# Kernel optimization log

Hardware: AMD Instinct MI355X
Metric: run time of the kernel (lower is better)

## Reference

```python
import jax, jax.numpy as jnp
import numpy as np

DIM = 768
NUM_HEADS = 12
HEAD_DIM = DIM // NUM_HEADS  # 64
IMG_W = 32
IMG_H = 32
B = 16
N = IMG_W * IMG_H + 1  # 1025 (CLS + grid)


def setup_inputs() -> dict:
    key = jax.random.key(0)
    k1, k2, k3, k4, k5 = jax.random.split(key, 5)
    x = jax.random.normal(k1, (B, N, DIM), dtype=jnp.float32)
    W_qkv = jax.random.normal(k2, (3 * DIM, DIM), dtype=jnp.float32) * 0.02
    W_proj = jax.random.normal(k3, (DIM, DIM), dtype=jnp.float32) * 0.02
    b_proj = jax.random.normal(k4, (DIM,), dtype=jnp.float32) * 0.02
    # learned mixed-RoPE frequencies, shape (2, num_heads * head_dim//2)
    freqs = jax.random.normal(k5, (2, NUM_HEADS * (HEAD_DIM // 2)), dtype=jnp.float32) * 0.1
    return {"x": x, "W_qkv": W_qkv, "W_proj": W_proj, "b_proj": b_proj, "freqs": freqs}


def _mixed_angles(freqs):
    # t_x = t % W, t_y = t // W over the flattened grid (init_t_xy)
    t = jnp.arange(IMG_W * IMG_H, dtype=jnp.float32)
    t_x = t % IMG_W
    t_y = jnp.floor(t / IMG_W)
    # outer products -> (N-1, H, hd/2) -> (H, N-1, hd/2); angle = fx + fy
    fx = (t_x[:, None] * freqs[0][None, :]).reshape(-1, NUM_HEADS, HEAD_DIM // 2)
    fy = (t_y[:, None] * freqs[1][None, :]).reshape(-1, NUM_HEADS, HEAD_DIM // 2)
    return (fx + fy).transpose(1, 0, 2)  # (H, N-1, hd/2)


def _apply_rope(t, cos, sin):
    # t: (B, H, N-1, hd); complex multiply on (even, odd) pairs
    pairs = t.reshape(*t.shape[:-1], HEAD_DIM // 2, 2)
    x0, x1 = pairs[..., 0], pairs[..., 1]
    o0 = x0 * cos - x1 * sin
    o1 = x0 * sin + x1 * cos
    return jnp.stack([o0, o1], axis=-1).reshape(t.shape)


def reference(x, W_qkv, W_proj, b_proj, freqs):
    Bx, Nx, C = x.shape
    scale = HEAD_DIM ** -0.5
    qkv = jnp.einsum('bnc,dc->bnd', x, W_qkv)  # Linear, no bias
    qkv = qkv.reshape(Bx, Nx, 3, NUM_HEADS, HEAD_DIM).transpose(2, 0, 3, 1, 4)
    q, k, v = qkv[0], qkv[1], qkv[2]  # (B, H, N, hd)

    ang = _mixed_angles(freqs)  # (H, N-1, hd/2)
    cos, sin = jnp.cos(ang), jnp.sin(ang)  # broadcast over batch

    # rotate all tokens except the leading CLS token
    q = jnp.concatenate([q[:, :, :1], _apply_rope(q[:, :, 1:], cos, sin)], axis=2)
    k = jnp.concatenate([k[:, :, :1], _apply_rope(k[:, :, 1:], cos, sin)], axis=2)

    attn = jax.nn.softmax(jnp.einsum('bhqd,bhkd->bhqk', q * scale, k), axis=-1)
    out = jnp.einsum('bhqk,bhkd->bhqd', attn, v)  # (B, H, N, hd)
    out = out.transpose(0, 2, 1, 3).reshape(Bx, Nx, C)
    return out @ W_proj.T + b_proj
```

## Files before the change

kernel.cpp:

```cpp
#include <hip/hip_runtime.h>
#include <math.h>

#define DIM     768
#define NH      12
#define HD      64
#define NTOK    1025
#define BATCH   16
#define MTOT    (BATCH * NTOK)
#define QKVD    (3 * DIM)

typedef short  short8 __attribute__((ext_vector_type(8)));
typedef float  f32x4  __attribute__((ext_vector_type(4)));

typedef const __attribute__((address_space(1))) void gvoid_t;
typedef __attribute__((address_space(3)))       void lvoid_t;
#define GLD16(gsrc, ldst) __builtin_amdgcn_global_load_lds( \
    (gvoid_t*)(gsrc), (lvoid_t*)(ldst), 16, 0, 0)

static __device__ __forceinline__ unsigned int f2bf(float f) {
    unsigned int u = __float_as_uint(f);
    u += 0x7FFFu + ((u >> 16) & 1u);
    return u >> 16;
}

static __device__ __forceinline__ float red_sum(float x) {
    x += __shfl_xor(x, 16);
    x += __shfl_xor(x, 32);
    return x;
}

__device__ __forceinline__ void cvt8(const float* __restrict__ src,
                                     unsigned short* __restrict__ dst, int i) {
    float4 a = *(const float4*)(src + (size_t)i*8);
    float4 b = *(const float4*)(src + (size_t)i*8 + 4);
    uint4 pk;
    pk.x = f2bf(a.x) | (f2bf(a.y) << 16);
    pk.y = f2bf(a.z) | (f2bf(a.w) << 16);
    pk.z = f2bf(b.x) | (f2bf(b.y) << 16);
    pk.w = f2bf(b.z) | (f2bf(b.w) << 16);
    *(uint4*)(dst + (size_t)i*8) = pk;
}

__global__ __launch_bounds__(256) void cvt_bf16_kernel(
    const float* __restrict__ x, const float* __restrict__ Wq,
    const float* __restrict__ Wp,
    unsigned short* __restrict__ xb, unsigned short* __restrict__ Wqb,
    unsigned short* __restrict__ Wpb)
{
    const int stride = gridDim.x * blockDim.x;
    const int tid = blockIdx.x * blockDim.x + threadIdx.x;
    for (int i = tid; i < MTOT*DIM/8;  i += stride) cvt8(x,  xb,  i);
    for (int i = tid; i < QKVD*DIM/8;  i += stride) cvt8(Wq, Wqb, i);
    for (int i = tid; i < DIM*DIM/8;   i += stride) cvt8(Wp, Wpb, i);
}

__global__ __launch_bounds__(256) void rope_tab_kernel(
    const float* __restrict__ freqs, float2* __restrict__ tab)
{
    const int gid = blockIdx.x * 256 + threadIdx.x;
    const int p  = gid & 31;
    const int n1 = (gid >> 5) & 1023;
    const int h  = gid >> 15;
    const float tx = (float)(n1 & 31), ty = (float)(n1 >> 5);
    const float ang = tx * freqs[h*32 + p] + ty * freqs[384 + h*32 + p];
    float s, c;
    sincosf(ang, &s, &c);
    tab[gid] = make_float2(c, s);
}

__device__ __forceinline__ void gemm_core(
    const unsigned short* __restrict__ Wb,
    const unsigned short* __restrict__ Xb,
    int D0, int T0, int maxXrow,
    short* Ws, short* Xs, f32x4 acc[4][4], int tid)
{
    const int lane = tid & 63;
    const int wu   = __builtin_amdgcn_readfirstlane(tid >> 6);
    const int wr   = wu >> 1, wc = wu & 1;
    const int l4   = lane >> 4, l15 = lane & 15;

    const int srow = lane >> 3;
    const int schk = (lane & 7) ^ srow;
    const unsigned short* wsrc[4];
    const unsigned short* xsrc[4];
#pragma unroll
    for (int i = 0; i < 4; ++i) {
        int r = wu*32 + i*8 + srow;
        wsrc[i] = Wb + (size_t)(D0 + r) * DIM + schk*8;
        int xr = T0 + r; if (xr > maxXrow) xr = maxXrow;
        xsrc[i] = Xb + (size_t)xr * DIM + schk*8;
    }

    for (int kt = 0; kt < DIM/64; ++kt) {
        __syncthreads();
#pragma unroll
        for (int i = 0; i < 4; ++i) {
            GLD16(wsrc[i] + kt*64, &Ws[(wu*4 + i) * 512]);
            GLD16(xsrc[i] + kt*64, &Xs[(wu*4 + i) * 512]);
        }
        __syncthreads();

        short8 wf[4][2], xf[4][2];
#pragma unroll
        for (int f = 0; f < 4; ++f) {
            const int rw = wr*64 + f*16 + l15;
            const int rx = wc*64 + f*16 + l15;
#pragma unroll
            for (int kf = 0; kf < 2; ++kf) {
                wf[f][kf] = *(const short8*)&Ws[rw*64 + (((kf*4 + l4) ^ (rw & 7)) << 3)];
                xf[f][kf] = *(const short8*)&Xs[rx*64 + (((kf*4 + l4) ^ (rx & 7)) << 3)];
            }
        }
        __builtin_amdgcn_s_setprio(1);
#pragma unroll
        for (int kf = 0; kf < 2; ++kf)
#pragma unroll
            for (int fm = 0; fm < 4; ++fm)
#pragma unroll
                for (int fn = 0; fn < 4; ++fn)
                    acc[fm][fn] = __builtin_amdgcn_mfma_f32_16x16x32_bf16(
                        wf[fm][kf], xf[fn][kf], acc[fm][fn], 0, 0, 0);
        __builtin_amdgcn_s_setprio(0);
    }
}

__global__ __launch_bounds__(256) void qkv_gemm_kernel(
    const unsigned short* __restrict__ Wqb, const unsigned short* __restrict__ xb,
    const float2* __restrict__ tab,
    unsigned short* __restrict__ Qb, unsigned short* __restrict__ Kb,
    unsigned short* __restrict__ Vb)
{
    __shared__ __align__(16) short Ws[128*64];
    __shared__ __align__(16) short Xs[128*64];
    f32x4 acc[4][4] = {};
    const int tid = threadIdx.x;
    const int D0 = blockIdx.x * 128;
    const int T0 = blockIdx.y * 128;
    gemm_core(Wqb, xb, D0, T0, MTOT - 1, Ws, Xs, acc, tid);

    const int lane = tid & 63;
    const int wu = tid >> 6, wr = wu >> 1, wc = wu & 1;
    const int l4 = lane >> 4, l15 = lane & 15;
    const int which = D0 / DIM;
    unsigned short* dst = (which == 0) ? Qb : (which == 1) ? Kb : Vb;
    const float qs = (which == 0) ? 0.125f * 1.44269504089f : 1.f;

    unsigned bArr[4], nArr[4];
    bool vArr[4];
#pragma unroll
    for (int fn = 0; fn < 4; ++fn) {
        unsigned m = T0 + wc*64 + fn*16 + l15;
        vArr[fn] = m < MTOT;
        bArr[fn] = m / NTOK;
        nArr[fn] = m - bArr[fn]*NTOK;
    }
#pragma unroll
    for (int fm = 0; fm < 4; ++fm) {
        const int hcol = (D0 % DIM) + wr*64 + fm*16 + l4*4;
        const int h = hcol >> 6, dd = hcol & 63;
        const int p0 = dd >> 1;
#pragma unroll
        for (int fn = 0; fn < 4; ++fn) {
            if (!vArr[fn]) continue;
            f32x4 a = acc[fm][fn];
            const int n = nArr[fn];
            if (which < 2) {
                int n1 = n > 0 ? n - 1 : 0;
                float4 cs = *(const float4*)&tab[(size_t)(h*1024 + n1)*32 + p0];
                if (n == 0) cs = make_float4(1.f, 0.f, 1.f, 0.f);
                float e0 = a[0], od0 = a[1], e1 = a[2], od1 = a[3];
                a[0] = e0*cs.x - od0*cs.y;  a[1] = e0*cs.y + od0*cs.x;
                a[2] = e1*cs.z - od1*cs.w;  a[3] = e1*cs.w + od1*cs.z;
            }
            uint2 pk;
            pk.x = f2bf(a[0]*qs) | (f2bf(a[1]*qs) << 16);
            pk.y = f2bf(a[2]*qs) | (f2bf(a[3]*qs) << 16);
            *(uint2*)&dst[((size_t)(bArr[fn]*NH + h)*NTOK + n)*HD + dd] = pk;
        }
    }
}

__global__ __launch_bounds__(256) void attn_mfma_kernel(
    const unsigned short* __restrict__ Qb,
    const unsigned short* __restrict__ Kb,
    const unsigned short* __restrict__ Vb,
    unsigned short* __restrict__ Obf)
{
    __shared__ __align__(16) char KsR[2][8192];
    __shared__ __align__(16) char VtR[2][8192];
    __shared__ __align__(16) char PsR[4][4096];

    const int tid  = threadIdx.x;
    const int lane = tid & 63;
    const int w    = __builtin_amdgcn_readfirstlane(tid >> 6);
    const int l4   = lane >> 4, l15 = lane & 15, l7 = lane & 7;

    const int d    = blockIdx.x;
    const int xcd  = d & 7;
    const int s    = d >> 3;
    const int bh   = xcd * 24 + s / 9;
    const int q0   = (s % 9) * 128;
    const size_t base = (size_t)bh * NTOK * HD;

    short8 qf[2][2];
#pragma unroll
    for (int qg = 0; qg < 2; ++qg) {
        int qr = q0 + w*32 + qg*16 + l15;
        int qrc = qr < NTOK ? qr : NTOK - 1;
        qf[qg][0] = *(const short8*)(Qb + base + (size_t)qrc*HD + l4*8);
        qf[qg][1] = *(const short8*)(Qb + base + (size_t)qrc*HD + 32 + l4*8);
    }

    float lA = 0.f, lB = 0.f;
    f32x4 oA[4] = {}, oB[4] = {};

    const int ktokb = tid >> 3;
    const int kchk  = tid & 7;
    const int vtok  = ((tid & 7) << 3) | ((tid >> 3) & 7);
    const int vc    = vtok >> 3;
    const int vb2   = (vtok & 7) * 2;
    char* Pw = &PsR[w][0];

    uint4 vg[2];
#pragma unroll
    for (int i = 0; i < 2; ++i)
        vg[i] = *(const uint4*)(Vb + base + (size_t)vtok*HD + w*8 + i*32);
#pragma unroll
    for (int i = 0; i < 2; ++i) {
        int tok = ktokb + i*32;
        int sc = kchk ^ (tok & 7);
        GLD16(Kb + base + (size_t)tok*HD + sc*8, &KsR[0][w*1024 + i*4096]);
    }
#pragma unroll
    for (int i = 0; i < 2; ++i) {
        const int vd0 = w*8 + i*32;
        unsigned short vs[8];
        vs[0]=(unsigned short)vg[i].x; vs[1]=(unsigned short)(vg[i].x>>16);
        vs[2]=(unsigned short)vg[i].y; vs[3]=(unsigned short)(vg[i].y>>16);
        vs[4]=(unsigned short)vg[i].z; vs[5]=(unsigned short)(vg[i].z>>16);
        vs[6]=(unsigned short)vg[i].w; vs[7]=(unsigned short)(vg[i].w>>16);
#pragma unroll
        for (int j = 0; j < 8; ++j)
            *(unsigned short*)(&VtR[0][0] + (vd0+j)*128 + ((vc ^ j) << 4) + vb2) = vs[j];
    }
#pragma unroll
    for (int i = 0; i < 2; ++i) {
        int gv = 64 + vtok;
        vg[i] = (gv < NTOK)
            ? *(const uint4*)(Vb + base + (size_t)gv*HD + w*8 + i*32)
            : make_uint4(0,0,0,0);
    }

    for (int kt = 0; kt < 17; ++kt) {
        const int buf = kt & 1;
        __syncthreads();

        if (kt < 16) {
            const int nb = buf ^ 1;
#pragma unroll
            for (int i = 0; i < 2; ++i) {
                int tok = ktokb + i*32;
                int gk = (kt+1)*64 + tok; if (gk > NTOK-1) gk = NTOK-1;
                int sc = kchk ^ (tok & 7);
                GLD16(Kb + base + (size_t)gk*HD + sc*8, &KsR[nb][w*1024 + i*4096]);
            }
#pragma unroll
            for (int i = 0; i < 2; ++i) {
                const int vd0 = w*8 + i*32;
                unsigned short vs[8];
                vs[0]=(unsigned short)vg[i].x; vs[1]=(unsigned short)(vg[i].x>>16);
                vs[2]=(unsigned short)vg[i].y; vs[3]=(unsigned short)(vg[i].y>>16);
                vs[4]=(unsigned short)vg[i].z; vs[5]=(unsigned short)(vg[i].z>>16);
                vs[6]=(unsigned short)vg[i].w; vs[7]=(unsigned short)(vg[i].w>>16);
#pragma unroll
                for (int j = 0; j < 8; ++j)
                    *(unsigned short*)(&VtR[nb][0] + (vd0+j)*128 + ((vc ^ j) << 4) + vb2) = vs[j];
            }
            const int ktn = (kt+2 < 17) ? kt+2 : 16;
#pragma unroll
            for (int i = 0; i < 2; ++i) {
                int gv = ktn*64 + vtok;
                vg[i] = (gv < NTOK)
                    ? *(const uint4*)(Vb + base + (size_t)gv*HD + w*8 + i*32)
                    : make_uint4(0,0,0,0);
            }
        }

        f32x4 sA[4] = {}, sB[4] = {};
        __builtin_amdgcn_s_setprio(1);
#pragma unroll
        for (int tg = 0; tg < 4; ++tg) {
            const int row = tg*16 + l15;
            short8 ka0 = *(const short8*)(&KsR[buf][0] + row*128 + ((l4 ^ l7) << 4));
            short8 ka1 = *(const short8*)(&KsR[buf][0] + row*128 + (((4 + l4) ^ l7) << 4));
            sA[tg] = __builtin_amdgcn_mfma_f32_16x16x32_bf16(ka0, qf[0][0], sA[tg], 0,0,0);
            sA[tg] = __builtin_amdgcn_mfma_f32_16x16x32_bf16(ka1, qf[0][1], sA[tg], 0,0,0);
            sB[tg] = __builtin_amdgcn_mfma_f32_16x16x32_bf16(ka0, qf[1][0], sB[tg], 0,0,0);
            sB[tg] = __builtin_amdgcn_mfma_f32_16x16x32_bf16(ka1, qf[1][1], sB[tg], 0,0,0);
        }
        __builtin_amdgcn_s_setprio(0);

        float pA[16], pB[16];
        if (kt == 16) {
#pragma unroll
            for (int tg = 0; tg < 4; ++tg)
#pragma unroll
                for (int r = 0; r < 4; ++r) {
                    int tok = 1024 + tg*16 + l4*4 + r;
                    float sa = (tok > 1024) ? -3e38f : sA[tg][r];
                    float sb = (tok > 1024) ? -3e38f : sB[tg][r];
                    pA[tg*4+r] = __builtin_exp2f(sa);
                    pB[tg*4+r] = __builtin_exp2f(sb);
                }
        } else {
#pragma unroll
            for (int tg = 0; tg < 4; ++tg)
#pragma unroll
                for (int r = 0; r < 4; ++r) {
                    pA[tg*4+r] = __builtin_exp2f(sA[tg][r]);
                    pB[tg*4+r] = __builtin_exp2f(sB[tg][r]);
                }
        }
        float psA = 0.f, psB = 0.f;
#pragma unroll
        for (int i = 0; i < 16; ++i) { psA += pA[i]; psB += pB[i]; }
        lA += psA;
        lB += psB;

#pragma unroll
        for (int tg = 0; tg < 4; ++tg) {
            unsigned k0a, k1a, k0b, k1b;
            asm volatile("v_cvt_pk_bf16_f32 %0, %1, %2" : "=v"(k0a) : "v"(pA[tg*4+0]), "v"(pA[tg*4+1]));
            asm volatile("v_cvt_pk_bf16_f32 %0, %1, %2" : "=v"(k1a) : "v"(pA[tg*4+2]), "v"(pA[tg*4+3]));
            asm volatile("v_cvt_pk_bf16_f32 %0, %1, %2" : "=v"(k0b) : "v"(pB[tg*4+0]), "v"(pB[tg*4+1]));
            asm volatile("v_cvt_pk_bf16_f32 %0, %1, %2" : "=v"(k1b) : "v"(pB[tg*4+2]), "v"(pB[tg*4+3]));
            const int chk = (((tg*2 + (l4 >> 1)) ^ l7) << 4) + (l4 & 1)*8;
            *(uint2*)(Pw + l15*128      + chk) = make_uint2(k0a, k1a);
            *(uint2*)(Pw + (16+l15)*128 + chk) = make_uint2(k0b, k1b);
        }
        __builtin_amdgcn_wave_barrier();

        const short8 pf00 = *(const short8*)(Pw + l15*128      + ((l4 ^ l7) << 4));
        const short8 pf01 = *(const short8*)(Pw + l15*128      + (((4+l4) ^ l7) << 4));
        const short8 pf10 = *(const short8*)(Pw + (16+l15)*128 + ((l4 ^ l7) << 4));
        const short8 pf11 = *(const short8*)(Pw + (16+l15)*128 + (((4+l4) ^ l7) << 4));

        __builtin_amdgcn_s_setprio(1);
#pragma unroll
        for (int dg = 0; dg < 4; ++dg) {
            const int dd = dg*16 + l15;
            short8 v0 = *(const short8*)(&VtR[buf][0] + dd*128 + ((l4 ^ (dd & 7)) << 4));
            short8 v1 = *(const short8*)(&VtR[buf][0] + dd*128 + (((4 + l4) ^ (dd & 7)) << 4));
            oA[dg] = __builtin_amdgcn_mfma_f32_16x16x32_bf16(v0, pf00, oA[dg], 0,0,0);
            oA[dg] = __builtin_amdgcn_mfma_f32_16x16x32_bf16(v1, pf01, oA[dg], 0,0,0);
            oB[dg] = __builtin_amdgcn_mfma_f32_16x16x32_bf16(v0, pf10, oB[dg], 0,0,0);
            oB[dg] = __builtin_amdgcn_mfma_f32_16x16x32_bf16(v1, pf11, oB[dg], 0,0,0);
        }
        __builtin_amdgcn_s_setprio(0);
    }

    const float liA = 1.f / red_sum(lA);
    const float liB = 1.f / red_sum(lB);
    const int b = bh / NH, h = bh % NH;
    const int qA = q0 + w*32 + l15;
    const int qB = qA + 16;
    if (qA < NTOK) {
        unsigned short* p = Obf + ((size_t)b*NTOK + qA)*DIM + h*HD + l4*4;
#pragma unroll
        for (int dg = 0; dg < 4; ++dg) {
            uint2 pk;
            pk.x = f2bf(oA[dg][0]*liA) | (f2bf(oA[dg][1]*liA) << 16);
            pk.y = f2bf(oA[dg][2]*liA) | (f2bf(oA[dg][3]*liA) << 16);
            *(uint2*)(p + dg*16) = pk;
        }
    }
    if (qB < NTOK) {
        unsigned short* p = Obf + ((size_t)b*NTOK + qB)*DIM + h*HD + l4*4;
#pragma unroll
        for (int dg = 0; dg < 4; ++dg) {
            uint2 pk;
            pk.x = f2bf(oB[dg][0]*liB) | (f2bf(oB[dg][1]*liB) << 16);
            pk.y = f2bf(oB[dg][2]*liB) | (f2bf(oB[dg][3]*liB) << 16);
            *(uint2*)(p + dg*16) = pk;
        }
    }
}

__global__ __launch_bounds__(256) void proj_gemm_kernel(
    const unsigned short* __restrict__ Wpb, const unsigned short* __restrict__ Obf,
    const float* __restrict__ bp, float* __restrict__ out)
{
    __shared__ __align__(16) short Ws[128*64];
    __shared__ __align__(16) short Xs[128*64];
    f32x4 acc[4][4] = {};
    const int tid = threadIdx.x;
    const int D0 = blockIdx.x * 128;
    const int T0 = blockIdx.y * 128;
    gemm_core(Wpb, Obf, D0, T0, MTOT - 1, Ws, Xs, acc, tid);

    const int lane = tid & 63;
    const int wu = tid >> 6, wr = wu >> 1, wc = wu & 1;
    const int l4 = lane >> 4, l15 = lane & 15;

    unsigned mArr[4];
    bool vArr[4];
#pragma unroll
    for (int fn = 0; fn < 4; ++fn) {
        unsigned m = T0 + wc*64 + fn*16 + l15;
        mArr[fn] = m;
        vArr[fn] = m < MTOT;
    }
#pragma unroll
    for (int fm = 0; fm < 4; ++fm) {
        const int nG = D0 + wr*64 + fm*16 + l4*4;
        const float4 bias = *(const float4*)&bp[nG];
#pragma unroll
        for (int fn = 0; fn < 4; ++fn) {
            if (!vArr[fn]) continue;
            f32x4 a = acc[fm][fn];
            float4 v = make_float4(a[0]+bias.x, a[1]+bias.y, a[2]+bias.z, a[3]+bias.w);
            *(float4*)&out[(size_t)mArr[fn]*DIM + nG] = v;
        }
    }
}

extern "C" void kernel_launch(void* const* d_in, const int* in_sizes, int n_in,
                              void* d_out, int out_size, void* d_ws, size_t ws_size,
                              hipStream_t stream)
{
    const float* x     = (const float*)d_in[0];
    const float* Wqkv  = (const float*)d_in[1];
    const float* Wp    = (const float*)d_in[2];
    const float* bp    = (const float*)d_in[3];
    const float* freqs = (const float*)d_in[4];
    float* out = (float*)d_out;

    const size_t SZ = (size_t)BATCH * NH * NTOK * HD;
    unsigned short* Qb  = (unsigned short*)d_ws;
    unsigned short* Kb  = Qb + SZ;
    unsigned short* Vb  = Kb + SZ;
    unsigned short* Obf = Vb + SZ;
    unsigned short* xb  = Obf + SZ;
    unsigned short* Wqb = xb + SZ;
    unsigned short* Wpb = Wqb + (size_t)QKVD * DIM;
    float2*         tab = (float2*)(Wpb + (size_t)DIM * DIM);

    cvt_bf16_kernel<<<2048, 256, 0, stream>>>(x, Wqkv, Wp, xb, Wqb, Wpb);
    rope_tab_kernel<<<1536, 256, 0, stream>>>(freqs, tab);
    qkv_gemm_kernel<<<dim3(QKVD/128, (MTOT + 127)/128), 256, 0, stream>>>(
        Wqb, xb, tab, Qb, Kb, Vb);
    attn_mfma_kernel<<<1728, 256, 0, stream>>>(Qb, Kb, Vb, Obf);
    proj_gemm_kernel<<<dim3(DIM/128, (MTOT + 127)/128), 256, 0, stream>>>(
        Wpb, Obf, bp, out);
}
```

Before: 279.6 us.

## Pad Q/K/V token dimension to 1088 with zeros to drop attention tail masking

```diff
diff --git a/kernel.cpp b/kernel.cpp
--- a/kernel.cpp
+++ b/kernel.cpp
@@ -5,6 +5,7 @@
 #define NH      12
 #define HD      64
 #define NTOK    1025
+#define NTOKP   1088
 #define BATCH   16
 #define MTOT    (BATCH * NTOK)
 #define QKVD    (3 * DIM)
@@ -66,6 +67,19 @@
     float s, c;
     sincosf(ang, &s, &c);
     tab[gid] = make_float2(c, s);
+}
+
+__global__ __launch_bounds__(256) void pad_zero_kernel(
+    unsigned short* __restrict__ Qb, unsigned short* __restrict__ Kb,
+    unsigned short* __restrict__ Vb)
+{
+    const int gid   = blockIdx.x * 256 + threadIdx.x;
+    const int which = gid / 96768;
+    const int r     = gid - which * 96768;
+    const int bh    = r / 504;
+    const int off   = r - bh * 504;
+    unsigned short* p = (which == 0) ? Qb : (which == 1) ? Kb : Vb;
+    *(uint4*)(p + ((size_t)bh*NTOKP + NTOK)*HD + off*8) = make_uint4(0,0,0,0);
 }
 
 __device__ __forceinline__ void gemm_core(
@@ -175,7 +189,7 @@
             uint2 pk;
             pk.x = f2bf(a[0]*qs) | (f2bf(a[1]*qs) << 16);
             pk.y = f2bf(a[2]*qs) | (f2bf(a[3]*qs) << 16);
-            *(uint2*)&dst[((size_t)(bArr[fn]*NH + h)*NTOK + n)*HD + dd] = pk;
+            *(uint2*)&dst[((size_t)(bArr[fn]*NH + h)*NTOKP + n)*HD + dd] = pk;
         }
     }
 }
@@ -186,8 +200,8 @@
     const unsigned short* __restrict__ Vb,
     unsigned short* __restrict__ Obf)
 {
-    __shared__ __align__(16) char KsR[2][8192];
-    __shared__ __align__(16) char VtR[2][8192];
+    __shared__ __align__(16) char KsR[2*8192];
+    __shared__ __align__(16) char VtR[2*8192];
     __shared__ __align__(16) char PsR[4][4096];
 
     const int tid  = threadIdx.x;
@@ -200,7 +214,7 @@
     const int s    = d >> 3;
     const int bh   = xcd * 24 + s / 9;
     const int q0   = (s % 9) * 128;
-    const size_t base = (size_t)bh * NTOK * HD;
+    const size_t base = (size_t)bh * NTOKP * HD;
 
     short8 qf[2][2];
 #pragma unroll
@@ -221,16 +235,19 @@
     const int vb2   = (vtok & 7) * 2;
     char* Pw = &PsR[w][0];
 
+    const unsigned short* kp0 = Kb + base + (size_t)ktokb*HD
+                                + (size_t)(kchk ^ (ktokb & 7))*8;
+    const unsigned short* kp1 = kp0 + 32*HD;
+    const unsigned short* vp  = Vb + base + (size_t)vtok*HD + w*8;
+
+    GLD16(kp0, KsR + w*1024);
+    GLD16(kp1, KsR + 4096 + w*1024);
+    kp0 += 4096; kp1 += 4096;
+
     uint4 vg[2];
-#pragma unroll
-    for (int i = 0; i < 2; ++i)
-        vg[i] = *(const uint4*)(Vb + base + (size_t)vtok*HD + w*8 + i*32);
-#pragma unroll
-    for (int i = 0; i < 2; ++i) {
-        int tok = ktokb + i*32;
-        int sc = kchk ^ (tok & 7);
-        GLD16(Kb + base + (size_t)tok*HD + sc*8, &KsR[0][w*1024 + i*4096]);
-    }
+    vg[0] = *(const uint4*)vp;
+    vg[1] = *(const uint4*)(vp + 32);
+    vp += 4096;
 #pragma unroll
     for (int i = 0; i < 2; ++i) {
         const int vd0 = w*8 + i*32;
@@ -241,29 +258,24 @@
         vs[6]=(unsigned short)vg[i].w; vs[7]=(unsigned short)(vg[i].w>>16);
 #pragma unroll
         for (int j = 0; j < 8; ++j)
-            *(unsigned short*)(&VtR[0][0] + (vd0+j)*128 + ((vc ^ j) << 4) + vb2) = vs[j];
-    }
-#pragma unroll
-    for (int i = 0; i < 2; ++i) {
-        int gv = 64 + vtok;
-        vg[i] = (gv < NTOK)
-            ? *(const uint4*)(Vb + base + (size_t)gv*HD + w*8 + i*32)
-            : make_uint4(0,0,0,0);
-    }
+            *(unsigned short*)(VtR + (vd0+j)*128 + ((vc ^ j) << 4) + vb2) = vs[j];
+    }
+    vg[0] = *(const uint4*)vp;
+    vg[1] = *(const uint4*)(vp + 32);
+    vp += 4096;
 
     for (int kt = 0; kt < 17; ++kt) {
         const int buf = kt & 1;
+        const char* Kc = KsR + buf*8192;
+        const char* Vc = VtR + buf*8192;
         __syncthreads();
 
         if (kt < 16) {
-            const int nb = buf ^ 1;
-#pragma unroll
-            for (int i = 0; i < 2; ++i) {
-                int tok = ktokb + i*32;
-                int gk = (kt+1)*64 + tok; if (gk > NTOK-1) gk = NTOK-1;
-                int sc = kchk ^ (tok & 7);
-                GLD16(Kb + base + (size_t)gk*HD + sc*8, &KsR[nb][w*1024 + i*4096]);
-            }
+            char* kd = KsR + (buf^1)*8192 + w*1024;
+            GLD16(kp0, kd);
+            GLD16(kp1, kd + 4096);
+            kp0 += 4096; kp1 += 4096;
+            char* vd = VtR + (buf^1)*8192;
 #pragma unroll
             for (int i = 0; i < 2; ++i) {
                 const int vd0 = w*8 + i*32;
@@ -274,15 +286,12 @@
                 vs[6]=(unsigned short)vg[i].w; vs[7]=(unsigned short)(vg[i].w>>16);
 #pragma unroll
                 for (int j = 0; j < 8; ++j)
-                    *(unsigned short*)(&VtR[nb][0] + (vd0+j)*128 + ((vc ^ j) << 4) + vb2) = vs[j];
+                    *(unsigned short*)(vd + (vd0+j)*128 + ((vc ^ j) << 4) + vb2) = vs[j];
             }
-            const int ktn = (kt+2 < 17) ? kt+2 : 16;
-#pragma unroll
-            for (int i = 0; i < 2; ++i) {
-                int gv = ktn*64 + vtok;
-                vg[i] = (gv < NTOK)
-                    ? *(const uint4*)(Vb + base + (size_t)gv*HD + w*8 + i*32)
-                    : make_uint4(0,0,0,0);
+            if (kt < 15) {
+                vg[0] = *(const uint4*)vp;
+                vg[1] = *(const uint4*)(vp + 32);
+                vp += 4096;
             }
         }
 
@@ -291,8 +300,8 @@
 #pragma unroll
         for (int tg = 0; tg < 4; ++tg) {
             const int row = tg*16 + l15;
-            short8 ka0 = *(const short8*)(&KsR[buf][0] + row*128 + ((l4 ^ l7) << 4));
-            short8 ka1 = *(const short8*)(&KsR[buf][0] + row*128 + (((4 + l4) ^ l7) << 4));
+            short8 ka0 = *(const short8*)(Kc + row*128 + ((l4 ^ l7) << 4));
+            short8 ka1 = *(const short8*)(Kc + row*128 + (((4 + l4) ^ l7) << 4));
             sA[tg] = __builtin_amdgcn_mfma_f32_16x16x32_bf16(ka0, qf[0][0], sA[tg], 0,0,0);
             sA[tg] = __builtin_amdgcn_mfma_f32_16x16x32_bf16(ka1, qf[0][1], sA[tg], 0,0,0);
             sB[tg] = __builtin_amdgcn_mfma_f32_16x16x32_bf16(ka0, qf[1][0], sB[tg], 0,0,0);
@@ -301,29 +310,14 @@
         __builtin_amdgcn_s_setprio(0);
 
         float pA[16], pB[16];
-        if (kt == 16) {
-#pragma unroll
-            for (int tg = 0; tg < 4; ++tg)
-#pragma unroll
-                for (int r = 0; r < 4; ++r) {
-                    int tok = 1024 + tg*16 + l4*4 + r;
-                    float sa = (tok > 1024) ? -3e38f : sA[tg][r];
-                    float sb = (tok > 1024) ? -3e38f : sB[tg][r];
-                    pA[tg*4+r] = __builtin_exp2f(sa);
-                    pB[tg*4+r] = __builtin_exp2f(sb);
-                }
-        } else {
-#pragma unroll
-            for (int tg = 0; tg < 4; ++tg)
-#pragma unroll
-                for (int r = 0; r < 4; ++r) {
-                    pA[tg*4+r] = __builtin_exp2f(sA[tg][r]);
-                    pB[tg*4+r] = __builtin_exp2f(sB[tg][r]);
-                }
-        }
         float psA = 0.f, psB = 0.f;
 #pragma unroll
-        for (int i = 0; i < 16; ++i) { psA += pA[i]; psB += pB[i]; }
+        for (int tg = 0; tg < 4; ++tg)
+#pragma unroll
+            for (int r = 0; r < 4; ++r) {
+                pA[tg*4+r] = __builtin_exp2f(sA[tg][r]); psA += pA[tg*4+r];
+                pB[tg*4+r] = __builtin_exp2f(sB[tg][r]); psB += pB[tg*4+r];
+            }
         lA += psA;
         lB += psB;
 
@@ -349,8 +343,8 @@
 #pragma unroll
         for (int dg = 0; dg < 4; ++dg) {
             const int dd = dg*16 + l15;
-            short8 v0 = *(const short8*)(&VtR[buf][0] + dd*128 + ((l4 ^ (dd & 7)) << 4));
-            short8 v1 = *(const short8*)(&VtR[buf][0] + dd*128 + (((4 + l4) ^ (dd & 7)) << 4));
+            short8 v0 = *(const short8*)(Vc + dd*128 + ((l4 ^ (dd & 7)) << 4));
+            short8 v1 = *(const short8*)(Vc + dd*128 + (((4 + l4) ^ (dd & 7)) << 4));
             oA[dg] = __builtin_amdgcn_mfma_f32_16x16x32_bf16(v0, pf00, oA[dg], 0,0,0);
             oA[dg] = __builtin_amdgcn_mfma_f32_16x16x32_bf16(v1, pf01, oA[dg], 0,0,0);
             oB[dg] = __builtin_amdgcn_mfma_f32_16x16x32_bf16(v0, pf10, oB[dg], 0,0,0);
@@ -359,8 +353,8 @@
         __builtin_amdgcn_s_setprio(0);
     }
 
-    const float liA = 1.f / red_sum(lA);
-    const float liB = 1.f / red_sum(lB);
+    const float liA = 1.f / (red_sum(lA) - 63.f);
+    const float liB = 1.f / (red_sum(lB) - 63.f);
     const int b = bh / NH, h = bh % NH;
     const int qA = q0 + w*32 + l15;
     const int qB = qA + 16;
@@ -435,11 +429,12 @@
     const float* freqs = (const float*)d_in[4];
     float* out = (float*)d_out;
 
-    const size_t SZ = (size_t)BATCH * NH * NTOK * HD;
+    const size_t SZP = (size_t)BATCH * NH * NTOKP * HD;
+    const size_t SZ  = (size_t)BATCH * NH * NTOK  * HD;
     unsigned short* Qb  = (unsigned short*)d_ws;
-    unsigned short* Kb  = Qb + SZ;
-    unsigned short* Vb  = Kb + SZ;
-    unsigned short* Obf = Vb + SZ;
+    unsigned short* Kb  = Qb + SZP;
+    unsigned short* Vb  = Kb + SZP;
+    unsigned short* Obf = Vb + SZP;
     unsigned short* xb  = Obf + SZ;
     unsigned short* Wqb = xb + SZ;
     unsigned short* Wpb = Wqb + (size_t)QKVD * DIM;
@@ -447,6 +442,7 @@
 
     cvt_bf16_kernel<<<2048, 256, 0, stream>>>(x, Wqkv, Wp, xb, Wqb, Wpb);
     rope_tab_kernel<<<1536, 256, 0, stream>>>(freqs, tab);
+    pad_zero_kernel<<<1134, 256, 0, stream>>>(Qb, Kb, Vb);
     qkv_gemm_kernel<<<dim3(QKVD/128, (MTOT + 127)/128), 256, 0, stream>>>(
         Wqb, xb, tab, Qb, Kb, Vb);
     attn_mfma_kernel<<<1728, 256, 0, stream>>>(Qb, Kb, Vb, Obf);
```

After: 297.1 us. 1.06x slower.

## Load V via async global-to-LDS and read transposed with ds_read_b64_tr_b16

Applied to the files above, without the earlier changes.

```diff
diff --git a/kernel.cpp b/kernel.cpp
--- a/kernel.cpp
+++ b/kernel.cpp
@@ -9,11 +9,13 @@
 #define MTOT    (BATCH * NTOK)
 #define QKVD    (3 * DIM)
 
-typedef short  short8 __attribute__((ext_vector_type(8)));
-typedef float  f32x4  __attribute__((ext_vector_type(4)));
+typedef short  short8  __attribute__((ext_vector_type(8)));
+typedef short  short4v __attribute__((ext_vector_type(4)));
+typedef float  f32x4   __attribute__((ext_vector_type(4)));
 
 typedef const __attribute__((address_space(1))) void gvoid_t;
 typedef __attribute__((address_space(3)))       void lvoid_t;
+typedef __attribute__((address_space(3)))       char lchar_t;
 #define GLD16(gsrc, ldst) __builtin_amdgcn_global_load_lds( \
     (gvoid_t*)(gsrc), (lvoid_t*)(ldst), 16, 0, 0)
 
@@ -216,40 +218,21 @@
 
     const int ktokb = tid >> 3;
     const int kchk  = tid & 7;
-    const int vtok  = ((tid & 7) << 3) | ((tid >> 3) & 7);
-    const int vc    = vtok >> 3;
-    const int vb2   = (vtok & 7) * 2;
+    const int c0 = tid, c1 = tid + 256;
+    const int vt0 = ((c0 >> 5) << 2) | ((c0 >> 1) & 3);
+    const int vt1 = ((c1 >> 5) << 2) | ((c1 >> 1) & 3);
+    const int vo0 = (((c0 >> 3) & 3) << 4) | ((c0 & 1) << 3);
+    const int vo1 = (((c1 >> 3) & 3) << 4) | ((c1 & 1) << 3);
     char* Pw = &PsR[w][0];
 
-    uint4 vg[2];
-#pragma unroll
-    for (int i = 0; i < 2; ++i)
-        vg[i] = *(const uint4*)(Vb + base + (size_t)vtok*HD + w*8 + i*32);
 #pragma unroll
     for (int i = 0; i < 2; ++i) {
         int tok = ktokb + i*32;
         int sc = kchk ^ (tok & 7);
         GLD16(Kb + base + (size_t)tok*HD + sc*8, &KsR[0][w*1024 + i*4096]);
     }
-#pragma unroll
-    for (int i = 0; i < 2; ++i) {
-        const int vd0 = w*8 + i*32;
-        unsigned short vs[8];
-        vs[0]=(unsigned short)vg[i].x; vs[1]=(unsigned short)(vg[i].x>>16);
-        vs[2]=(unsigned short)vg[i].y; vs[3]=(unsigned short)(vg[i].y>>16);
-        vs[4]=(unsigned short)vg[i].z; vs[5]=(unsigned short)(vg[i].z>>16);
-        vs[6]=(unsigned short)vg[i].w; vs[7]=(unsigned short)(vg[i].w>>16);
-#pragma unroll
-        for (int j = 0; j < 8; ++j)
-            *(unsigned short*)(&VtR[0][0] + (vd0+j)*128 + ((vc ^ j) << 4) + vb2) = vs[j];
-    }
-#pragma unroll
-    for (int i = 0; i < 2; ++i) {
-        int gv = 64 + vtok;
-        vg[i] = (gv < NTOK)
-            ? *(const uint4*)(Vb + base + (size_t)gv*HD + w*8 + i*32)
-            : make_uint4(0,0,0,0);
-    }
+    GLD16(Vb + base + (size_t)vt0*HD + vo0, &VtR[0][w*1024]);
+    GLD16(Vb + base + (size_t)vt1*HD + vo1, &VtR[0][4096 + w*1024]);
 
     for (int kt = 0; kt < 17; ++kt) {
         const int buf = kt & 1;
@@ -264,26 +247,10 @@
                 int sc = kchk ^ (tok & 7);
                 GLD16(Kb + base + (size_t)gk*HD + sc*8, &KsR[nb][w*1024 + i*4096]);
             }
-#pragma unroll
-            for (int i = 0; i < 2; ++i) {
-                const int vd0 = w*8 + i*32;
-                unsigned short vs[8];
-                vs[0]=(unsigned short)vg[i].x; vs[1]=(unsigned short)(vg[i].x>>16);
-                vs[2]=(unsigned short)vg[i].y; vs[3]=(unsigned short)(vg[i].y>>16);
-                vs[4]=(unsigned short)vg[i].z; vs[5]=(unsigned short)(vg[i].z>>16);
-                vs[6]=(unsigned short)vg[i].w; vs[7]=(unsigned short)(vg[i].w>>16);
-#pragma unroll
-                for (int j = 0; j < 8; ++j)
-                    *(unsigned short*)(&VtR[nb][0] + (vd0+j)*128 + ((vc ^ j) << 4) + vb2) = vs[j];
-            }
-            const int ktn = (kt+2 < 17) ? kt+2 : 16;
-#pragma unroll
-            for (int i = 0; i < 2; ++i) {
-                int gv = ktn*64 + vtok;
-                vg[i] = (gv < NTOK)
-                    ? *(const uint4*)(Vb + base + (size_t)gv*HD + w*8 + i*32)
-                    : make_uint4(0,0,0,0);
-            }
+            int g0 = (kt+1)*64 + vt0; if (g0 > NTOK-1) g0 = NTOK-1;
+            int g1 = (kt+1)*64 + vt1; if (g1 > NTOK-1) g1 = NTOK-1;
+            GLD16(Vb + base + (size_t)g0*HD + vo0, &VtR[nb][w*1024]);
+            GLD16(Vb + base + (size_t)g1*HD + vo1, &VtR[nb][4096 + w*1024]);
         }
 
         f32x4 sA[4] = {}, sB[4] = {};
@@ -345,18 +312,70 @@
         const short8 pf10 = *(const short8*)(Pw + (16+l15)*128 + ((l4 ^ l7) << 4));
         const short8 pf11 = *(const short8*)(Pw + (16+l15)*128 + (((4+l4) ^ l7) << 4));
 
-        __builtin_amdgcn_s_setprio(1);
-#pragma unroll
-        for (int dg = 0; dg < 4; ++dg) {
-            const int dd = dg*16 + l15;
-            short8 v0 = *(const short8*)(&VtR[buf][0] + dd*128 + ((l4 ^ (dd & 7)) << 4));
-            short8 v1 = *(const short8*)(&VtR[buf][0] + dd*128 + (((4 + l4) ^ (dd & 7)) << 4));
-            oA[dg] = __builtin_amdgcn_mfma_f32_16x16x32_bf16(v0, pf00, oA[dg], 0,0,0);
-            oA[dg] = __builtin_amdgcn_mfma_f32_16x16x32_bf16(v1, pf01, oA[dg], 0,0,0);
-            oB[dg] = __builtin_amdgcn_mfma_f32_16x16x32_bf16(v0, pf10, oB[dg], 0,0,0);
-            oB[dg] = __builtin_amdgcn_mfma_f32_16x16x32_bf16(v1, pf11, oB[dg], 0,0,0);
-        }
-        __builtin_amdgcn_s_setprio(0);
+        const unsigned trb = (unsigned)(unsigned long long)
+            (lchar_t*)(&VtR[buf][0] + (l4 << 10) + (l15 << 3));
+        short4v r0a, r0b, r1a, r1b, r2a, r2b, r3a, r3b;
+
+        asm volatile(
+            "ds_read_b64_tr_b16 %0, %8 offset:0\n\t"
+            "ds_read_b64_tr_b16 %1, %8 offset:512\n\t"
+            "ds_read_b64_tr_b16 %2, %8 offset:128\n\t"
+            "ds_read_b64_tr_b16 %3, %8 offset:640\n\t"
+            "ds_read_b64_tr_b16 %4, %8 offset:256\n\t"
+            "ds_read_b64_tr_b16 %5, %8 offset:768\n\t"
+            "ds_read_b64_tr_b16 %6, %8 offset:384\n\t"
+            "ds_read_b64_tr_b16 %7, %8 offset:896\n\t"
+            "s_waitcnt lgkmcnt(0)"
+            : "=&v"(r0a), "=&v"(r0b), "=&v"(r1a), "=&v"(r1b),
+              "=&v"(r2a), "=&v"(r2b), "=&v"(r3a), "=&v"(r3b)
+            : "v"(trb) : "memory");
+        __builtin_amdgcn_sched_barrier(0);
+        {
+            short8 v0 = __builtin_shufflevector(r0a, r0b, 0,1,2,3,4,5,6,7);
+            short8 v1 = __builtin_shufflevector(r1a, r1b, 0,1,2,3,4,5,6,7);
+            short8 v2 = __builtin_shufflevector(r2a, r2b, 0,1,2,3,4,5,6,7);
+            short8 v3 = __builtin_shufflevector(r3a, r3b, 0,1,2,3,4,5,6,7);
+            __builtin_amdgcn_s_setprio(1);
+            oA[0] = __builtin_amdgcn_mfma_f32_16x16x32_bf16(v0, pf00, oA[0], 0,0,0);
+            oB[0] = __builtin_amdgcn_mfma_f32_16x16x32_bf16(v0, pf10, oB[0], 0,0,0);
+            oA[1] = __builtin_amdgcn_mfma_f32_16x16x32_bf16(v1, pf00, oA[1], 0,0,0);
+            oB[1] = __builtin_amdgcn_mfma_f32_16x16x32_bf16(v1, pf10, oB[1], 0,0,0);
+            oA[2] = __builtin_amdgcn_mfma_f32_16x16x32_bf16(v2, pf00, oA[2], 0,0,0);
+            oB[2] = __builtin_amdgcn_mfma_f32_16x16x32_bf16(v2, pf10, oB[2], 0,0,0);
+            oA[3] = __builtin_amdgcn_mfma_f32_16x16x32_bf16(v3, pf00, oA[3], 0,0,0);
+            oB[3] = __builtin_amdgcn_mfma_f32_16x16x32_bf16(v3, pf10, oB[3], 0,0,0);
+            __builtin_amdgcn_s_setprio(0);
+        }
+        asm volatile(
+            "ds_read_b64_tr_b16 %0, %8 offset:4096\n\t"
+            "ds_read_b64_tr_b16 %1, %8 offset:4608\n\t"
+            "ds_read_b64_tr_b16 %2, %8 offset:4224\n\t"
+            "ds_read_b64_tr_b16 %3, %8 offset:4736\n\t"
+            "ds_read_b64_tr_b16 %4, %8 offset:4352\n\t"
+            "ds_read_b64_tr_b16 %5, %8 offset:4864\n\t"
+            "ds_read_b64_tr_b16 %6, %8 offset:4480\n\t"
+            "ds_read_b64_tr_b16 %7, %8 offset:4992\n\t"
+            "s_waitcnt lgkmcnt(0)"
+            : "=&v"(r0a), "=&v"(r0b), "=&v"(r1a), "=&v"(r1b),
+              "=&v"(r2a), "=&v"(r2b), "=&v"(r3a), "=&v"(r3b)
+            : "v"(trb) : "memory");
+        __builtin_amdgcn_sched_barrier(0);
+        {
+            short8 v0 = __builtin_shufflevector(r0a, r0b, 0,1,2,3,4,5,6,7);
+            short8 v1 = __builtin_shufflevector(r1a, r1b, 0,1,2,3,4,5,6,7);
+            short8 v2 = __builtin_shufflevector(r2a, r2b, 0,1,2,3,4,5,6,7);
+            short8 v3 = __builtin_shufflevector(r3a, r3b, 0,1,2,3,4,5,6,7);
+            __builtin_amdgcn_s_setprio(1);
+            oA[0] = __builtin_amdgcn_mfma_f32_16x16x32_bf16(v0, pf01, oA[0], 0,0,0);
+            oB[0] = __builtin_amdgcn_mfma_f32_16x16x32_bf16(v0, pf11, oB[0], 0,0,0);
+            oA[1] = __builtin_amdgcn_mfma_f32_16x16x32_bf16(v1, pf01, oA[1], 0,0,0);
+            oB[1] = __builtin_amdgcn_mfma_f32_16x16x32_bf16(v1, pf11, oB[1], 0,0,0);
+            oA[2] = __builtin_amdgcn_mfma_f32_16x16x32_bf16(v2, pf01, oA[2], 0,0,0);
+            oB[2] = __builtin_amdgcn_mfma_f32_16x16x32_bf16(v2, pf11, oB[2], 0,0,0);
+            oA[3] = __builtin_amdgcn_mfma_f32_16x16x32_bf16(v3, pf01, oA[3], 0,0,0);
+            oB[3] = __builtin_amdgcn_mfma_f32_16x16x32_bf16(v3, pf11, oB[3], 0,0,0);
+            __builtin_amdgcn_s_setprio(0);
+        }
     }
 
     const float liA = 1.f / red_sum(lA);
```

After: 271.1 us. 3.0% less time.
